# Kernel optimization log

Hardware: AMD Instinct MI355X
Metric: run time of the kernel (lower is better)

The kernel has to match this reference:

```python
import jax, jax.numpy as jnp
import numpy as np

NUM_USERS = 100_000
NUM_ITEMS = 50_000
N_TOTAL = 150_100
EMBED_DIM = 64
NUM_LAYERS = 3
N_EDGES = 3_000_000
BATCH = 4096


def setup_inputs() -> dict:
    key = jax.random.key(0)
    k1, k2, k3, k4, k5, k6 = jax.random.split(key, 6)
    node_emb = jax.random.normal(k1, (N_TOTAL, EMBED_DIM), dtype=jnp.float32) * 0.1
    # COO sparse normalized adjacency (static irregular pattern)
    adj_row = jax.random.randint(k2, (N_EDGES,), 0, N_TOTAL, dtype=jnp.int32)
    adj_col = jax.random.randint(k3, (N_EDGES,), 0, N_TOTAL, dtype=jnp.int32)
    adj_val = jax.random.uniform(k4, (N_EDGES,), dtype=jnp.float32) * 0.05
    user_ids = jax.random.randint(k5, (BATCH,), 0, NUM_USERS, dtype=jnp.int32)
    item_ids = jax.random.randint(k6, (BATCH,), 0, NUM_ITEMS, dtype=jnp.int32)
    return {"node_emb": node_emb, "adj_val": adj_val, "adj_row": adj_row,
            "adj_col": adj_col, "user_ids": user_ids, "item_ids": item_ids}


def reference(node_emb, adj_val, adj_row, adj_col, user_ids, item_ids):
    # LightGCN propagation: K sparse SpMM layers, running mean over K+1 embeddings
    emb = node_emb                       # [N, D] layer-0
    acc = emb                            # running sum instead of stack+mean
    for _ in range(NUM_LAYERS):
        # SpMM: out[r] += val * emb[c]   (COO scatter-add)
        msgs = adj_val[:, None] * emb[adj_col]          # [E, D]
        emb = jax.ops.segment_sum(msgs, adj_row, num_segments=N_TOTAL)
        acc = acc + emb
    final = acc / jnp.float32(NUM_LAYERS + 1)           # mean over layers
    users = final[:NUM_USERS]
    items = final[NUM_USERS:NUM_USERS + NUM_ITEMS]
    u = users[user_ids]                                 # [B, D]
    i = items[item_ids]                                 # [B, D]
    return (u * i).sum(axis=-1)                         # [B]
```

## Files before the change

### kernel.cpp

```cpp
#include <hip/hip_runtime.h>

#define N_TOTAL    150100
#define NUM_USERS  100000
#define DIM        64
#define BSHIFT     8
#define BROWS      (1 << BSHIFT)
#define NBUK       ((N_TOTAL + BROWS - 1) / BROWS)
#define EPB        4096
#define EPT        16
#define CAP        5632
#define RSP        260

#define VSCALE     262144.0f
#define VINV       (1.0f / 262144.0f)

__device__ __forceinline__ int wave_incl_scan(int x, int lane) {
    #pragma unroll
    for (int off = 1; off < 64; off <<= 1) {
        int y = __shfl_up(x, off, 64);
        if (lane >= off) x += y;
    }
    return x;
}

__device__ __forceinline__ float ub0(unsigned w) { return (float)(w & 0xFFu); }
__device__ __forceinline__ float ub1(unsigned w) { return (float)((w >> 8) & 0xFFu); }
__device__ __forceinline__ float ub2(unsigned w) { return (float)((w >> 16) & 0xFFu); }
__device__ __forceinline__ float ub3(unsigned w) { return (float)(w >> 24); }

__device__ __forceinline__ unsigned quant_pack(float4 f, float inv) {
    int a = __float2int_rn(f.x * inv) + 128;
    int b = __float2int_rn(f.y * inv) + 128;
    int c = __float2int_rn(f.z * inv) + 128;
    int d = __float2int_rn(f.w * inv) + 128;
    a = min(max(a, 0), 255); b = min(max(b, 0), 255);
    c = min(max(c, 0), 255); d = min(max(d, 0), 255);
    return (unsigned)a | ((unsigned)b << 8) | ((unsigned)c << 16) | ((unsigned)d << 24);
}

__global__ void convert_quant(const float4* __restrict__ in4,
                              unsigned* __restrict__ q, float* __restrict__ sc,
                              int* __restrict__ gcount) {
    int t = blockIdx.x * blockDim.x + threadIdx.x;
    if (t < NBUK) gcount[t] = 0;
    int r = t >> 4, sl = t & 15;
    if (r >= N_TOTAL) return;
    float4 f = in4[(size_t)r * 16 + sl];
    float m = fmaxf(fmaxf(fabsf(f.x), fabsf(f.y)), fmaxf(fabsf(f.z), fabsf(f.w)));
    #pragma unroll
    for (int off = 1; off < 16; off <<= 1) m = fmaxf(m, __shfl_xor(m, off, 64));
    float inv = (m > 1e-30f) ? 127.0f / m : 0.0f;
    q[(size_t)r * 16 + sl] = quant_pack(f, inv);
    if (sl == 0) sc[r] = m * (1.0f / 127.0f);
}

__global__ void __launch_bounds__(256, 4) fill_buckets(
        const int* __restrict__ rows, const int* __restrict__ cols,
        const float* __restrict__ vals, int n_edges,
        int* __restrict__ gcount,
        uint2* __restrict__ epk8) {
    __shared__ unsigned      payb[EPB];
    __shared__ unsigned char rowb[EPB];
    __shared__ short         tgtb[EPB];
    __shared__ int hist[NBUK];
    __shared__ int pref[NBUK];
    __shared__ int cur[NBUK];
    __shared__ int loc[NBUK];
    __shared__ int wtot[4];
    const int tid = threadIdx.x;
    const int lane = tid & 63, wid = tid >> 6;
    const int base = blockIdx.x * EPB;
    int end = base + EPB; if (end > n_edges) end = n_edges;
    const int cnt = end - base;

    for (int i = tid; i < NBUK; i += 256) hist[i] = 0;

    unsigned pay[EPT];
    unsigned er[EPT];
    __syncthreads();

    if (cnt == EPB) {
        #pragma unroll
        for (int g = 0; g < 4; ++g) {
            const int e = base + (g * 256 + tid) * 4;
            int4   r4 = *(const int4*)(rows + e);
            int4   c4 = *(const int4*)(cols + e);
            float4 v4 = *(const float4*)(vals + e);
            int rr[4] = { r4.x, r4.y, r4.z, r4.w };
            int cc[4] = { c4.x, c4.y, c4.z, c4.w };
            float vv[4] = { v4.x, v4.y, v4.z, v4.w };
            #pragma unroll
            for (int k = 0; k < 4; ++k) {
                const int j = g * 4 + k;
                int q = (int)(vv[k] * VSCALE + 0.5f);
                if (q > 16383) q = 16383;
                pay[j] = ((unsigned)cc[k] << 14) | (unsigned)q;
                er[j]  = (unsigned)rr[k];
                atomicAdd(&hist[rr[k] >> BSHIFT], 1);
            }
        }
    } else {
        #pragma unroll
        for (int g = 0; g < 4; ++g) {
            const int e0 = base + (g * 256 + tid) * 4;
            #pragma unroll
            for (int k = 0; k < 4; ++k) {
                const int j = g * 4 + k;
                const int e = e0 + k;
                if (e < end) {
                    int r = rows[e];
                    int q = (int)(vals[e] * VSCALE + 0.5f);
                    if (q > 16383) q = 16383;
                    pay[j] = ((unsigned)cols[e] << 14) | (unsigned)q;
                    er[j]  = (unsigned)r;
                    atomicAdd(&hist[r >> BSHIFT], 1);
                } else {
                    er[j] = 0xFFFFFFFFu;
                }
            }
        }
    }
    __syncthreads();

    for (int b = tid; b < NBUK; b += 256) {
        int h = hist[b];
        loc[b] = h ? atomicAdd(&gcount[b], h) : 0;
    }
    const int t0 = tid * 3;
    int t1 = t0 + 3; if (t1 > NBUK) t1 = NBUK;
    int s = 0;
    for (int i = t0; i < t1; ++i) s += hist[i];
    int incl = wave_incl_scan(s, lane);
    if (lane == 63) wtot[wid] = incl;
    __syncthreads();
    int wofs = 0;
    for (int w = 0; w < wid; ++w) wofs += wtot[w];
    int run = incl + wofs - s;
    for (int i = t0; i < t1; ++i) {
        int h = hist[i];
        pref[i] = run;
        cur[i] = run;
        run += h;
    }
    __syncthreads();

    #pragma unroll
    for (int j = 0; j < EPT; ++j) {
        unsigned r = er[j];
        if (r != 0xFFFFFFFFu) {
            int b = (int)(r >> BSHIFT);
            int pos = atomicAdd(&cur[b], 1);
            payb[pos] = pay[j];
            rowb[pos] = (unsigned char)(r & (BROWS - 1));
            tgtb[pos] = (short)b;
        }
    }
    __syncthreads();

    for (int i = tid; i < cnt; i += 256) {
        int b = tgtb[i];
        int o = loc[b] + (i - pref[b]);
        if (o < CAP) {
            epk8[(size_t)b * CAP + o] = make_uint2(payb[i], (unsigned)rowb[i]);
        }
    }
}

__global__ void __launch_bounds__(256) bucket_sort(
        uint2* __restrict__ epk8,
        const int* __restrict__ gcount,
        int* __restrict__ rs) {
    __shared__ unsigned      buf[CAP];
    __shared__ unsigned char rbuf[CAP];
    __shared__ int hist[BROWS];
    __shared__ int curl[BROWS];
    __shared__ int wtot[4];
    const int tid = threadIdx.x;
    const int lane = tid & 63, wid = tid >> 6;
    const int b = blockIdx.x;
    const size_t k0 = (size_t)b * CAP;
    int cnt = gcount[b]; if (cnt > CAP) cnt = CAP;

    hist[tid] = 0;
    __syncthreads();
    for (int i = tid; i < cnt; i += 256) {
        uint2 e = epk8[k0 + i];
        buf[i]  = e.x;
        rbuf[i] = (unsigned char)e.y;
        atomicAdd(&hist[e.y & 255u], 1);
    }
    __syncthreads();
    int s = hist[tid];
    int incl = wave_incl_scan(s, lane);
    if (lane == 63) wtot[wid] = incl;
    __syncthreads();
    int wofs = 0;
    for (int w = 0; w < wid; ++w) wofs += wtot[w];
    int ex = incl + wofs - s;
    const int rbase = b << BSHIFT;
    int nrow = N_TOTAL - rbase; if (nrow > BROWS) nrow = BROWS;
    const int o0 = 2 * b * CAP;
    if (tid < nrow) rs[b * RSP + tid] = o0 + ex;
    if (tid == 0) rs[b * RSP + nrow] = o0 + cnt;
    curl[tid] = ex;
    __syncthreads();
    unsigned* out = (unsigned*)epk8;
    for (int i = tid; i < cnt; i += 256) {
        int rl = rbuf[i];
        int pos = atomicAdd(&curl[rl], 1);
        out[o0 + pos] = buf[i];
    }
}

__device__ __forceinline__ void rowsum8(const unsigned* __restrict__ qt,
                                        const float* __restrict__ sc,
                                        const int* __restrict__ rs,
                                        const unsigned* __restrict__ epk,
                                        int r, int sl, int subbase,
                                        float4& sA, float4& sB) {
    const int* rsb = rs + (r >> BSHIFT) * RSP + (r & (BROWS - 1));
    int k0 = rsb[0], k1 = rsb[1];
    sA = make_float4(0.f, 0.f, 0.f, 0.f);
    sB = make_float4(0.f, 0.f, 0.f, 0.f);
    float corr = 0.f;
    const unsigned* qrow = qt + (sl << 1);
    unsigned pr = epk[k0 + sl];
    if (sl >= k1 - k0) pr = 0u;
    float vsl = (float)(pr & 16383u) * VINV * sc[pr >> 14];
    for (int kb = k0; kb < k1; kb += 8) {
        unsigned prn = epk[kb + 8 + sl];
        corr += vsl;
        #pragma unroll
        for (int j = 0; j < 8; ++j) {
            unsigned e = (unsigned)__shfl((int)pr, subbase + j, 64);
            float vs = __shfl(vsl, subbase + j, 64);
            int c = (int)(e >> 14);
            uint2 w = *(const uint2*)(qrow + ((size_t)c << 4));
            sA.x += vs * ub0(w.x); sA.y += vs * ub1(w.x);
            sA.z += vs * ub2(w.x); sA.w += vs * ub3(w.x);
            sB.x += vs * ub0(w.y); sB.y += vs * ub1(w.y);
            sB.z += vs * ub2(w.y); sB.w += vs * ub3(w.y);
        }
        if (sl >= k1 - (kb + 8)) prn = 0u;
        vsl = (float)(prn & 16383u) * VINV * sc[prn >> 14];
        pr = prn;
    }
    corr += __shfl_xor(corr, 1, 64);
    corr += __shfl_xor(corr, 2, 64);
    corr += __shfl_xor(corr, 4, 64);
    float c128 = 128.0f * corr;
    sA.x -= c128; sA.y -= c128; sA.z -= c128; sA.w -= c128;
    sB.x -= c128; sB.y -= c128; sB.z -= c128; sB.w -= c128;
}

__global__ void spmm_q8(const unsigned* __restrict__ qt,
                        const float* __restrict__ sc,
                        const int* __restrict__ rs,
                        const unsigned* __restrict__ epk,
                        unsigned* __restrict__ qo,
                        float* __restrict__ so) {
    int t = blockIdx.x * blockDim.x + threadIdx.x;
    int r = t >> 3;
    int sl = t & 7;
    int lane = threadIdx.x & 63;
    int subbase = lane & 56;
    if (r >= N_TOTAL) return;
    float4 sA, sB;
    rowsum8(qt, sc, rs, epk, r, sl, subbase, sA, sB);
    float mA = fmaxf(fmaxf(fabsf(sA.x), fabsf(sA.y)), fmaxf(fabsf(sA.z), fabsf(sA.w)));
    float mB = fmaxf(fmaxf(fabsf(sB.x), fabsf(sB.y)), fmaxf(fabsf(sB.z), fabsf(sB.w)));
    float m = fmaxf(mA, mB);
    m = fmaxf(m, __shfl_xor(m, 1, 64));
    m = fmaxf(m, __shfl_xor(m, 2, 64));
    m = fmaxf(m, __shfl_xor(m, 4, 64));
    float inv = (m > 1e-30f) ? 127.0f / m : 0.0f;
    uint2 o = make_uint2(quant_pack(sA, inv), quant_pack(sB, inv));
    *(uint2*)(qo + (size_t)r * 16 + (sl << 1)) = o;
    if (sl == 0) so[r] = m * (1.0f / 127.0f);
}

__device__ __forceinline__ float4 dec4(unsigned w, float s) {
    return make_float4(s * (ub0(w) - 128.0f), s * (ub1(w) - 128.0f),
                       s * (ub2(w) - 128.0f), s * (ub3(w) - 128.0f));
}

__global__ void final_dot_fused(const float4* __restrict__ emb4,
                                const unsigned* __restrict__ q1,
                                const float* __restrict__ s1,
                                const unsigned* __restrict__ q2,
                                const float* __restrict__ s2,
                                const int* __restrict__ rs,
                                const unsigned* __restrict__ epk,
                                const int* __restrict__ user_ids,
                                const int* __restrict__ item_ids,
                                float* __restrict__ out, int batch) {
    int t = blockIdx.x * blockDim.x + threadIdx.x;
    int p = t >> 4;
    int h = (t >> 3) & 1;
    int sl = t & 7;
    int lane = threadIdx.x & 63;
    int subbase = lane & 56;
    if (p >= batch) return;
    int r = h ? (NUM_USERS + item_ids[p]) : user_ids[p];

    float4 lA, lB;
    rowsum8(q2, s2, rs, epk, r, sl, subbase, lA, lB);

    float4 n0 = emb4[(size_t)r * 16 + (sl << 1)];
    float4 n1 = emb4[(size_t)r * 16 + (sl << 1) + 1];
    uint2 aw = *(const uint2*)(q1 + (size_t)r * 16 + (sl << 1));
    uint2 bw = *(const uint2*)(q2 + (size_t)r * 16 + (sl << 1));
    float sa = s1[r], sb = s2[r];
    float4 a0 = dec4(aw.x, sa), a1 = dec4(aw.y, sa);
    float4 b0 = dec4(bw.x, sb), b1 = dec4(bw.y, sb);

    float f0 = n0.x + a0.x + b0.x + lA.x;
    float f1 = n0.y + a0.y + b0.y + lA.y;
    float f2 = n0.z + a0.z + b0.z + lA.z;
    float f3 = n0.w + a0.w + b0.w + lA.w;
    float f4 = n1.x + a1.x + b1.x + lB.x;
    float f5 = n1.y + a1.y + b1.y + lB.y;
    float f6 = n1.z + a1.z + b1.z + lB.z;
    float f7 = n1.w + a1.w + b1.w + lB.w;

    float s = f0 * __shfl_xor(f0, 8, 64)
            + f1 * __shfl_xor(f1, 8, 64)
            + f2 * __shfl_xor(f2, 8, 64)
            + f3 * __shfl_xor(f3, 8, 64)
            + f4 * __shfl_xor(f4, 8, 64)
            + f5 * __shfl_xor(f5, 8, 64)
            + f6 * __shfl_xor(f6, 8, 64)
            + f7 * __shfl_xor(f7, 8, 64);
    s += __shfl_xor(s, 1, 64);
    s += __shfl_xor(s, 2, 64);
    s += __shfl_xor(s, 4, 64);
    if ((t & 15) == 0) out[p] = s * (1.0f / 16.0f);
}


static inline size_t align256(size_t x) { return (x + 255) & ~(size_t)255; }

extern "C" void kernel_launch(void* const* d_in, const int* in_sizes, int n_in,
                              void* d_out, int out_size, void* d_ws, size_t ws_size,
                              hipStream_t stream) {
    const float* node_emb = (const float*)d_in[0];
    const float* adj_val  = (const float*)d_in[1];
    const int*   adj_row  = (const int*)d_in[2];
    const int*   adj_col  = (const int*)d_in[3];
    const int*   user_ids = (const int*)d_in[4];
    const int*   item_ids = (const int*)d_in[5];
    float* out = (float*)d_out;

    const int n_edges = in_sizes[1];
    const int batch   = in_sizes[4];

    const size_t qtab_bytes = (size_t)N_TOTAL * 16 * sizeof(unsigned);
    const size_t sc_bytes   = (size_t)N_TOTAL * sizeof(float);

    char* p = (char*)d_ws;
    size_t off = 0;
    unsigned* q0 = (unsigned*)(p + off); off = align256(off + qtab_bytes);
    unsigned* q1 = (unsigned*)(p + off); off = align256(off + qtab_bytes);
    unsigned* q2 = (unsigned*)(p + off); off = align256(off + qtab_bytes);
    float* s0    = (float*)(p + off);    off = align256(off + sc_bytes);
    float* s1    = (float*)(p + off);    off = align256(off + sc_bytes);
    float* s2    = (float*)(p + off);    off = align256(off + sc_bytes);
    int* gcount  = (int*)(p + off);      off = align256(off + (size_t)NBUK * sizeof(int));
    int* rs      = (int*)(p + off);      off = align256(off + (size_t)NBUK * RSP * sizeof(int));
    uint2* epk8  = (uint2*)(p + off);    off = align256(off + (size_t)NBUK * CAP * sizeof(uint2));
    (void)ws_size;

    const int nbf = (n_edges + EPB - 1) / EPB;
    const int rblocks = ((N_TOTAL * 16) + 255) / 256;
    const int sblocks = ((N_TOTAL * 8) + 255) / 256;

    convert_quant<<<rblocks, 256, 0, stream>>>(
        (const float4*)node_emb, q0, s0, gcount);

    fill_buckets<<<nbf, 256, 0, stream>>>(adj_row, adj_col, adj_val, n_edges,
                                          gcount, epk8);
    bucket_sort<<<NBUK, 256, 0, stream>>>(epk8, gcount, rs);

    const unsigned* epk = (const unsigned*)epk8;

    spmm_q8<<<sblocks, 256, 0, stream>>>(q0, s0, rs, epk, q1, s1);
    spmm_q8<<<sblocks, 256, 0, stream>>>(q1, s1, rs, epk, q2, s2);

    {
        int threads = batch * 16;
        final_dot_fused<<<(threads + 255) / 256, 256, 0, stream>>>(
            (const float4*)node_emb, q1, s1, q2, s2, rs, epk,
            user_ids, item_ids, out, batch);
    }
}
```

Measured before the change: 260.5 us.

## Fuse quant conversion into fill kernel and use nontemporal loads/stores

Merges the embedding quantization kernel and the edge bucket-fill kernel into a single launch by block-index partitioning, and zeroes the bucket counters with a memset instead. It also switches the edge scratch buffers, the sorted edge stream and the quantized outputs to nontemporal loads and stores to reduce cache pollution. This saves one kernel launch and lets the two independent phases overlap. The risk is that conversion blocks now share the fill kernel's shared-memory footprint and launch bounds, and nontemporal hints on data that gets reused (the epk reads in the SpMM layers) may hurt caching.

```diff
diff --git a/kernel.cpp b/kernel.cpp
--- a/kernel.cpp
+++ b/kernel.cpp
@@ -10,6 +10,7 @@
 #define EPT        16
 #define CAP        5632
 #define RSP        260
+#define CONVBLKS   ((N_TOTAL * 16 + 255) / 256)
 
 #define VSCALE     262144.0f
 #define VINV       (1.0f / 262144.0f)
@@ -38,27 +39,26 @@
     return (unsigned)a | ((unsigned)b << 8) | ((unsigned)c << 16) | ((unsigned)d << 24);
 }
 
-__global__ void convert_quant(const float4* __restrict__ in4,
-                              unsigned* __restrict__ q, float* __restrict__ sc,
-                              int* __restrict__ gcount) {
-    int t = blockIdx.x * blockDim.x + threadIdx.x;
-    if (t < NBUK) gcount[t] = 0;
-    int r = t >> 4, sl = t & 15;
-    if (r >= N_TOTAL) return;
-    float4 f = in4[(size_t)r * 16 + sl];
-    float m = fmaxf(fmaxf(fabsf(f.x), fabsf(f.y)), fmaxf(fabsf(f.z), fabsf(f.w)));
-    #pragma unroll
-    for (int off = 1; off < 16; off <<= 1) m = fmaxf(m, __shfl_xor(m, off, 64));
-    float inv = (m > 1e-30f) ? 127.0f / m : 0.0f;
-    q[(size_t)r * 16 + sl] = quant_pack(f, inv);
-    if (sl == 0) sc[r] = m * (1.0f / 127.0f);
-}
-
-__global__ void __launch_bounds__(256, 4) fill_buckets(
+__global__ void __launch_bounds__(256, 4) conv_fill(
+        const float4* __restrict__ in4,
+        unsigned* __restrict__ q, float* __restrict__ sc,
         const int* __restrict__ rows, const int* __restrict__ cols,
         const float* __restrict__ vals, int n_edges,
         int* __restrict__ gcount,
-        uint2* __restrict__ epk8) {
+        unsigned long long* __restrict__ epk8) {
+    if (blockIdx.x < CONVBLKS) {
+        int t = blockIdx.x * 256 + threadIdx.x;
+        int r = t >> 4, sl = t & 15;
+        if (r >= N_TOTAL) return;
+        float4 f = in4[(size_t)r * 16 + sl];
+        float m = fmaxf(fmaxf(fabsf(f.x), fabsf(f.y)), fmaxf(fabsf(f.z), fabsf(f.w)));
+        #pragma unroll
+        for (int off = 1; off < 16; off <<= 1) m = fmaxf(m, __shfl_xor(m, off, 64));
+        float inv = (m > 1e-30f) ? 127.0f / m : 0.0f;
+        q[(size_t)r * 16 + sl] = quant_pack(f, inv);
+        if (sl == 0) sc[r] = m * (1.0f / 127.0f);
+        return;
+    }
     __shared__ unsigned      payb[EPB];
     __shared__ unsigned char rowb[EPB];
     __shared__ short         tgtb[EPB];
@@ -69,7 +69,7 @@
     __shared__ int wtot[4];
     const int tid = threadIdx.x;
     const int lane = tid & 63, wid = tid >> 6;
-    const int base = blockIdx.x * EPB;
+    const int base = (blockIdx.x - CONVBLKS) * EPB;
     int end = base + EPB; if (end > n_edges) end = n_edges;
     const int cnt = end - base;
 
@@ -92,9 +92,9 @@
             #pragma unroll
             for (int k = 0; k < 4; ++k) {
                 const int j = g * 4 + k;
-                int q = (int)(vv[k] * VSCALE + 0.5f);
-                if (q > 16383) q = 16383;
-                pay[j] = ((unsigned)cc[k] << 14) | (unsigned)q;
+                int qv = (int)(vv[k] * VSCALE + 0.5f);
+                if (qv > 16383) qv = 16383;
+                pay[j] = ((unsigned)cc[k] << 14) | (unsigned)qv;
                 er[j]  = (unsigned)rr[k];
                 atomicAdd(&hist[rr[k] >> BSHIFT], 1);
             }
@@ -109,9 +109,9 @@
                 const int e = e0 + k;
                 if (e < end) {
                     int r = rows[e];
-                    int q = (int)(vals[e] * VSCALE + 0.5f);
-                    if (q > 16383) q = 16383;
-                    pay[j] = ((unsigned)cols[e] << 14) | (unsigned)q;
+                    int qv = (int)(vals[e] * VSCALE + 0.5f);
+                    if (qv > 16383) qv = 16383;
+                    pay[j] = ((unsigned)cols[e] << 14) | (unsigned)qv;
                     er[j]  = (unsigned)r;
                     atomicAdd(&hist[r >> BSHIFT], 1);
                 } else {
@@ -161,13 +161,15 @@
         int b = tgtb[i];
         int o = loc[b] + (i - pref[b]);
         if (o < CAP) {
-            epk8[(size_t)b * CAP + o] = make_uint2(payb[i], (unsigned)rowb[i]);
+            unsigned long long v =
+                ((unsigned long long)rowb[i] << 32) | (unsigned long long)payb[i];
+            __builtin_nontemporal_store(v, &epk8[(size_t)b * CAP + o]);
         }
     }
 }
 
 __global__ void __launch_bounds__(256) bucket_sort(
-        uint2* __restrict__ epk8,
+        unsigned long long* __restrict__ epk8,
         const int* __restrict__ gcount,
         int* __restrict__ rs) {
     __shared__ unsigned      buf[CAP];
@@ -184,10 +186,11 @@
     hist[tid] = 0;
     __syncthreads();
     for (int i = tid; i < cnt; i += 256) {
-        uint2 e = epk8[k0 + i];
-        buf[i]  = e.x;
-        rbuf[i] = (unsigned char)e.y;
-        atomicAdd(&hist[e.y & 255u], 1);
+        unsigned long long e = __builtin_nontemporal_load(&epk8[k0 + i]);
+        unsigned rl = (unsigned)(e >> 32);
+        buf[i]  = (unsigned)e;
+        rbuf[i] = (unsigned char)rl;
+        atomicAdd(&hist[rl & 255u], 1);
     }
     __syncthreads();
     int s = hist[tid];
@@ -208,7 +211,7 @@
     for (int i = tid; i < cnt; i += 256) {
         int rl = rbuf[i];
         int pos = atomicAdd(&curl[rl], 1);
-        out[o0 + pos] = buf[i];
+        __builtin_nontemporal_store(buf[i], &out[o0 + pos]);
     }
 }
 
@@ -224,11 +227,11 @@
     sB = make_float4(0.f, 0.f, 0.f, 0.f);
     float corr = 0.f;
     const unsigned* qrow = qt + (sl << 1);
-    unsigned pr = epk[k0 + sl];
+    unsigned pr = __builtin_nontemporal_load(&epk[k0 + sl]);
     if (sl >= k1 - k0) pr = 0u;
     float vsl = (float)(pr & 16383u) * VINV * sc[pr >> 14];
     for (int kb = k0; kb < k1; kb += 8) {
-        unsigned prn = epk[kb + 8 + sl];
+        unsigned prn = __builtin_nontemporal_load(&epk[kb + 8 + sl]);
         corr += vsl;
         #pragma unroll
         for (int j = 0; j < 8; ++j) {
@@ -274,8 +277,10 @@
     m = fmaxf(m, __shfl_xor(m, 2, 64));
     m = fmaxf(m, __shfl_xor(m, 4, 64));
     float inv = (m > 1e-30f) ? 127.0f / m : 0.0f;
-    uint2 o = make_uint2(quant_pack(sA, inv), quant_pack(sB, inv));
-    *(uint2*)(qo + (size_t)r * 16 + (sl << 1)) = o;
+    unsigned long long ov =
+        ((unsigned long long)quant_pack(sB, inv) << 32) |
+        (unsigned long long)quant_pack(sA, inv);
+    __builtin_nontemporal_store(ov, (unsigned long long*)(qo + (size_t)r * 16 + (sl << 1)));
     if (sl == 0) so[r] = m * (1.0f / 127.0f);
 }
 
@@ -367,18 +372,19 @@
     float* s2    = (float*)(p + off);    off = align256(off + sc_bytes);
     int* gcount  = (int*)(p + off);      off = align256(off + (size_t)NBUK * sizeof(int));
     int* rs      = (int*)(p + off);      off = align256(off + (size_t)NBUK * RSP * sizeof(int));
-    uint2* epk8  = (uint2*)(p + off);    off = align256(off + (size_t)NBUK * CAP * sizeof(uint2));
+    unsigned long long* epk8 = (unsigned long long*)(p + off);
+    off = align256(off + (size_t)NBUK * CAP * sizeof(unsigned long long));
     (void)ws_size;
 
     const int nbf = (n_edges + EPB - 1) / EPB;
-    const int rblocks = ((N_TOTAL * 16) + 255) / 256;
     const int sblocks = ((N_TOTAL * 8) + 255) / 256;
 
-    convert_quant<<<rblocks, 256, 0, stream>>>(
-        (const float4*)node_emb, q0, s0, gcount);
-
-    fill_buckets<<<nbf, 256, 0, stream>>>(adj_row, adj_col, adj_val, n_edges,
-                                          gcount, epk8);
+    hipMemsetAsync(gcount, 0, (size_t)NBUK * sizeof(int), stream);
+
+    conv_fill<<<CONVBLKS + nbf, 256, 0, stream>>>(
+        (const float4*)node_emb, q0, s0,
+        adj_row, adj_col, adj_val, n_edges, gcount, epk8);
+
     bucket_sort<<<NBUK, 256, 0, stream>>>(epk8, gcount, rs);
 
     const unsigned* epk = (const unsigned*)epk8;
```

After: 381.2 us. 46.3% more time.
